# Kernel tuning notes

Hardware: AMD Instinct MI355X
Metric: run time of the kernel (lower is better)

The kernel has to match this reference:

```python
import jax, jax.numpy as jnp
import numpy as np


def _nearest(x, h, w):
    # torch F.interpolate(mode='nearest'): src_idx = floor(dst_idx * in/out)
    Hi, Wi = x.shape[-2], x.shape[-1]
    ri = (jnp.arange(h) * Hi) // h
    ci = (jnp.arange(w) * Wi) // w
    return jnp.take(jnp.take(x, ri, axis=-2), ci, axis=-1)


def _conv2d(x, wgt, bias):
    y = jax.lax.conv_general_dilated(x, wgt, (1, 1), 'SAME',
                                     dimension_numbers=('NCHW', 'OIHW', 'NCHW'))
    return y + bias.reshape(1, -1, 1, 1)


def setup_inputs() -> dict:
    key = jax.random.key(0)
    ks = jax.random.split(key, 6)
    b, c, ref_n, h, w = 1, 128, 4, 64, 64
    Hv, Wv = 256, 256
    return {
        'feats_t': jax.random.normal(ks[0], (b, c, h, w), jnp.float32),
        'feats_ref': jax.random.normal(ks[1], (b, c, ref_n, h, w), jnp.float32),
        'v_t': jax.random.uniform(ks[2], (b, 1, Hv, Wv), dtype=jnp.float32),
        'v_ref': jax.random.uniform(ks[3], (b, 1, ref_n, Hv, Wv), dtype=jnp.float32),
        'conv1_w': jax.random.normal(ks[4], (1, 1, 3, 3), jnp.float32) * 0.1,
        'conv1_b': jnp.zeros((1,), jnp.float32),
        'conv2_w': jax.random.normal(ks[5], (1, 1, 3, 3), jnp.float32) * 0.1,
        'conv2_b': jnp.zeros((1,), jnp.float32),
    }


def reference(feats_t, feats_ref, v_t, v_ref, conv1_w, conv1_b, conv2_w, conv2_b):
    b, c, ref_n, h, w = feats_ref.shape
    # nearest-resize visibility masks to feature resolution
    vt = _nearest(v_t, h, w)                      # (b, 1, h, w)
    vr = _nearest(v_ref, h, w)                    # (b, 1, ref_n, h, w)
    ft = feats_t * vt                             # (b, c, h, w)
    fr = feats_ref * vr                           # (b, c, ref_n, h, w)
    # cost volume: corr[b,r,q,k] = sum_c ft[b,c,q] * fr[b,c,r,k]
    corr = jnp.einsum('bcq,bcrk->brqk',
                      ft.reshape(b, c, h * w),
                      fr.reshape(b, c, ref_n, h * w))
    corr = corr.reshape(b, ref_n, h, w, h, w)
    # separable 4D conv: 3x3 over (h_ref, w_ref), then 3x3 over (h_t, w_t)
    x = _conv2d(corr.reshape(b * ref_n * h * w, 1, h, w), conv1_w, conv1_b)
    x = x.reshape(b, ref_n, h, w, h, w).transpose(0, 1, 4, 5, 2, 3)
    x = _conv2d(x.reshape(b * ref_n * h * w, 1, h, w), conv2_w, conv2_b)
    corr = x.reshape(b, ref_n, h, w, h, w).transpose(0, 1, 4, 5, 2, 3)
    # softmax3d: joint softmax over (ref_n, h_ref, w_ref) per query location
    m = jnp.max(corr, axis=(1, 4, 5), keepdims=True)
    e = jnp.exp(corr - m)
    corr = e / jnp.sum(e, axis=(1, 4, 5), keepdims=True)
    # weighted aggregation: out[b,c,q] = sum_{r,k} fr[b,c,r,k] * corr[b,r,q,k]
    out = jnp.einsum('bcrk,brqk->bcq',
                     fr.reshape(b, c, ref_n, h * w),
                     corr.reshape(b, ref_n, h * w, h * w))
    return out.reshape(b, c, h, w)
```

## Files before the change

kernel.cpp:

```cpp
#include <hip/hip_runtime.h>
#include <stdint.h>
#include <math.h>

typedef short bf16x8 __attribute__((ext_vector_type(8)));
typedef float f32x16 __attribute__((ext_vector_type(16)));
typedef unsigned int uint4v __attribute__((ext_vector_type(4)));

#define GAS __attribute__((address_space(1)))
#define LAS __attribute__((address_space(3)))

#define CDIM 128
#define NQ   4096
#define NK   16384
#define QT   128
#define KTILE 64

__device__ __forceinline__ unsigned short f2bf(float f) {
    unsigned int u = __builtin_bit_cast(unsigned int, f);
    u = (u + 0x7fffu + ((u >> 16) & 1u)) >> 16;
    return (unsigned short)u;
}

__device__ __forceinline__ void gload_lds16(const void* g, void* l) {
    __builtin_amdgcn_global_load_lds((const GAS unsigned int*)g, (LAS unsigned int*)l, 16, 0, 0);
}

__device__ __forceinline__ unsigned cvtpk(float a, float b) {
    unsigned r;
    asm("v_cvt_pk_bf16_f32 %0, %1, %2" : "=v"(r) : "v"(a), "v"(b));
    return r;
}

__device__ __forceinline__ void swap32(unsigned& a, unsigned& b) {
    asm("v_permlane32_swap_b32 %0, %1" : "+v"(a), "+v"(b));
}

__global__ void prep_q_kernel(const float* __restrict__ feats_t,
                              const float* __restrict__ v_t,
                              const float* __restrict__ w2,
                              unsigned int* __restrict__ Q32) {
    int idx = blockIdx.x * 256 + threadIdx.x;
    int q = idx & 4095, cp = idx >> 12;
    int y = q >> 6, x = q & 63;
    const float* fb0 = feats_t + (size_t)(cp * 2) * 4096;
    const float* fb1 = fb0 + 4096;
    float wv[9];
#pragma unroll
    for (int i = 0; i < 9; ++i) wv[i] = w2[i];
    float acc0 = 0.f, acc1 = 0.f;
#pragma unroll
    for (int u = 0; u < 3; ++u) {
        int yy = y + u - 1;
        if ((unsigned)yy >= 64u) continue;
#pragma unroll
        for (int v = 0; v < 3; ++v) {
            int xx = x + v - 1;
            if ((unsigned)xx >= 64u) continue;
            float m = wv[u * 3 + v] * v_t[yy * 1024 + xx * 4];
            acc0 += m * fb0[yy * 64 + xx];
            acc1 += m * fb1[yy * 64 + xx];
        }
    }
    Q32[(size_t)q * 64 + cp] = (unsigned)f2bf(acc0) | ((unsigned)f2bf(acc1) << 16);
}

__global__ void prep_p_kernel(const float* __restrict__ feats_ref,
                              const float* __restrict__ v_ref,
                              float* __restrict__ P,
                              unsigned short* __restrict__ Vt2) {
    int idx = blockIdx.x * 256 + threadIdx.x;
    int c = idx >> 14, rk = idx & 16383;
    int r = rk >> 12, k4 = rk & 4095, ky = k4 >> 6, kx = k4 & 63;
    float v = feats_ref[idx] * v_ref[r * 65536 + ky * 1024 + kx * 4];
    P[idx] = v;
    Vt2[(size_t)(rk >> 6) * 8192 + (((rk >> 3) & 7) * 128 + c) * 8 + (rk & 7)] = f2bf(v);
}

__global__ void prep_k2_kernel(const float* __restrict__ P,
                               const float* __restrict__ w1,
                               unsigned int* __restrict__ K32) {
    int idx = blockIdx.x * 256 + threadIdx.x;
    int rk = idx & 16383, cp2 = idx >> 14;
    int r = rk >> 12, k4 = rk & 4095, ky = k4 >> 6, kx = k4 & 63;
    const float* pb0 = P + (size_t)(cp2 * 2) * NK + r * 4096;
    const float* pb1 = pb0 + NK;
    float wv[9];
#pragma unroll
    for (int i = 0; i < 9; ++i) wv[i] = w1[i];
    float acc0 = 0.f, acc1 = 0.f;
#pragma unroll
    for (int u = 0; u < 3; ++u) {
        int yy = ky + u - 1;
        if ((unsigned)yy >= 64u) continue;
#pragma unroll
        for (int v = 0; v < 3; ++v) {
            int xx = kx + v - 1;
            if ((unsigned)xx >= 64u) continue;
            float w = wv[u * 3 + v];
            acc0 += w * pb0[yy * 64 + xx];
            acc1 += w * pb1[yy * 64 + xx];
        }
    }
    int tile = rk >> 6, rw = rk & 63;
    K32[(size_t)tile * 4096 + ((cp2 >> 2) * 64 + rw) * 4 + (cp2 & 3)] =
        (unsigned)f2bf(acc0) | ((unsigned)f2bf(acc1) << 16);
}

template<int KS>
__launch_bounds__(256, 2)
__global__ void attn_kernel(const unsigned short* __restrict__ Qg,
                            const unsigned short* __restrict__ Kt,
                            const unsigned short* __restrict__ Vt2,
                            float* __restrict__ Opart,
                            float* __restrict__ lpart) {
    constexpr int NITER = (NK / KS) / KTILE;
    __shared__ __align__(16) unsigned short KV[2][2][8192];

    const int tid = threadIdx.x;
    const int wid = tid >> 6;
    const int lane = tid & 63;
    const int l31 = lane & 31;
    const int lh = lane >> 5;
    const int ks = blockIdx.x & (KS - 1);
    const int qt = blockIdx.x / KS;
    const int q0 = qt * QT + wid * 32;
    const int tile0 = ks * NITER;

    bf16x8 qf[8];
#pragma unroll
    for (int s = 0; s < 8; ++s)
        qf[s] = *(const bf16x8*)(Qg + (size_t)(q0 + l31) * CDIM + s * 16 + lh * 8);

    f32x16 accO[4];
#pragma unroll
    for (int u = 0; u < 4; ++u)
#pragma unroll
        for (int r = 0; r < 16; ++r) accO[u][r] = 0.f;
    float l_acc = 0.f;

#define STAGE(nb, tg)                                                             \
    do {                                                                          \
        _Pragma("unroll") for (int j = 0; j < 4; ++j) {                           \
            int mb = (wid * 4 + j) * 64;                                          \
            gload_lds16(Kt + (size_t)(tg) * 8192 + (mb + lane) * 8,               \
                        &KV[(nb)][0][mb * 8]);                                    \
            gload_lds16(Vt2 + (size_t)(tg) * 8192 + (mb + lane) * 8,              \
                        &KV[(nb)][1][mb * 8]);                                    \
        }                                                                         \
    } while (0)

    STAGE(0, tile0);

#pragma unroll 1
    for (int it = 0; it < NITER; ++it) {
        const int bc = it & 1;
        __syncthreads();
        if (it + 1 < NITER) {
            STAGE(bc ^ 1, tile0 + it + 1);
            asm volatile("s_waitcnt vmcnt(8)" ::: "memory");
        } else {
            asm volatile("s_waitcnt vmcnt(0)" ::: "memory");
        }
        __syncthreads();

        f32x16 S0, S1;
#pragma unroll
        for (int r = 0; r < 16; ++r) { S0[r] = 0.f; S1[r] = 0.f; }
        __builtin_amdgcn_s_setprio(1);
#pragma unroll
        for (int s = 0; s < 8; ++s) {
            bf16x8 kf0 = *(const bf16x8*)(&KV[bc][0][((s * 2 + lh) * 64 + l31) * 8]);
            S0 = __builtin_amdgcn_mfma_f32_32x32x16_bf16(kf0, qf[s], S0, 0, 0, 0);
        }
#pragma unroll
        for (int s = 0; s < 8; ++s) {
            bf16x8 kf1 = *(const bf16x8*)(&KV[bc][0][((s * 2 + lh) * 64 + 32 + l31) * 8]);
            S1 = __builtin_amdgcn_mfma_f32_32x32x16_bf16(kf1, qf[s], S1, 0, 0, 0);
        }
        __builtin_amdgcn_s_setprio(0);

        float e0[16];
#pragma unroll
        for (int r = 0; r < 16; ++r) e0[r] = __expf(S0[r]);
        {
            float t0 = (e0[0] + e0[1]) + (e0[2] + e0[3]);
            float t1 = (e0[4] + e0[5]) + (e0[6] + e0[7]);
            float t2 = (e0[8] + e0[9]) + (e0[10] + e0[11]);
            float t3 = (e0[12] + e0[13]) + (e0[14] + e0[15]);
            l_acc += (t0 + t1) + (t2 + t3);
        }
        unsigned a0 = cvtpk(e0[0], e0[1]),   a1 = cvtpk(e0[2], e0[3]);
        unsigned a2 = cvtpk(e0[4], e0[5]),   a3 = cvtpk(e0[6], e0[7]);
        unsigned a4 = cvtpk(e0[8], e0[9]),   a5 = cvtpk(e0[10], e0[11]);
        unsigned a6 = cvtpk(e0[12], e0[13]), a7 = cvtpk(e0[14], e0[15]);
        swap32(a0, a2); swap32(a1, a3); swap32(a4, a6); swap32(a5, a7);
        bf16x8 pA0 = __builtin_bit_cast(bf16x8, (uint4v){a0, a1, a2, a3});
        bf16x8 pB0 = __builtin_bit_cast(bf16x8, (uint4v){a4, a5, a6, a7});

        __builtin_amdgcn_s_setprio(1);
#pragma unroll
        for (int u = 0; u < 4; ++u) {
            bf16x8 v0a = *(const bf16x8*)(&KV[bc][1][((lh) * 128 + u * 32 + l31) * 8]);
            accO[u] = __builtin_amdgcn_mfma_f32_32x32x16_bf16(v0a, pA0, accO[u], 0, 0, 0);
            bf16x8 v0b = *(const bf16x8*)(&KV[bc][1][((2 + lh) * 128 + u * 32 + l31) * 8]);
            accO[u] = __builtin_amdgcn_mfma_f32_32x32x16_bf16(v0b, pB0, accO[u], 0, 0, 0);
        }
        __builtin_amdgcn_s_setprio(0);

        float e1[16];
#pragma unroll
        for (int r = 0; r < 16; ++r) e1[r] = __expf(S1[r]);
        {
            float t0 = (e1[0] + e1[1]) + (e1[2] + e1[3]);
            float t1 = (e1[4] + e1[5]) + (e1[6] + e1[7]);
            float t2 = (e1[8] + e1[9]) + (e1[10] + e1[11]);
            float t3 = (e1[12] + e1[13]) + (e1[14] + e1[15]);
            l_acc += (t0 + t1) + (t2 + t3);
        }
        unsigned b0 = cvtpk(e1[0], e1[1]),   b1 = cvtpk(e1[2], e1[3]);
        unsigned b2 = cvtpk(e1[4], e1[5]),   b3 = cvtpk(e1[6], e1[7]);
        unsigned b4 = cvtpk(e1[8], e1[9]),   b5 = cvtpk(e1[10], e1[11]);
        unsigned b6 = cvtpk(e1[12], e1[13]), b7 = cvtpk(e1[14], e1[15]);
        swap32(b0, b2); swap32(b1, b3); swap32(b4, b6); swap32(b5, b7);
        bf16x8 pA1 = __builtin_bit_cast(bf16x8, (uint4v){b0, b1, b2, b3});
        bf16x8 pB1 = __builtin_bit_cast(bf16x8, (uint4v){b4, b5, b6, b7});

        __builtin_amdgcn_s_setprio(1);
#pragma unroll
        for (int u = 0; u < 4; ++u) {
            bf16x8 v1a = *(const bf16x8*)(&KV[bc][1][((4 + lh) * 128 + u * 32 + l31) * 8]);
            accO[u] = __builtin_amdgcn_mfma_f32_32x32x16_bf16(v1a, pA1, accO[u], 0, 0, 0);
            bf16x8 v1b = *(const bf16x8*)(&KV[bc][1][((6 + lh) * 128 + u * 32 + l31) * 8]);
            accO[u] = __builtin_amdgcn_mfma_f32_32x32x16_bf16(v1b, pB1, accO[u], 0, 0, 0);
        }
        __builtin_amdgcn_s_setprio(0);
    }
#undef STAGE

    l_acc += __shfl_xor(l_acc, 32);
    if (lane < 32) lpart[ks * NQ + q0 + l31] = l_acc;
#pragma unroll
    for (int u = 0; u < 4; ++u)
#pragma unroll
        for (int r = 0; r < 16; ++r) {
            int c = u * 32 + (r & 3) + 8 * (r >> 2) + 4 * lh;
            Opart[((size_t)(ks * CDIM + c)) * NQ + q0 + l31] = accO[u][r];
        }
}

template<int KS>
__global__ void reduce_kernel(const float* __restrict__ Opart,
                              const float* __restrict__ lpart,
                              float* __restrict__ out) {
    int i = blockIdx.x * 256 + threadIdx.x;
    int c = i >> 12, q = i & 4095;
    float den = 0.f, o = 0.f;
#pragma unroll
    for (int s = 0; s < KS; ++s) {
        den += lpart[s * NQ + q];
        o += Opart[((size_t)(s * CDIM + c)) * NQ + q];
    }
    out[(size_t)c * NQ + q] = o / den;
}

extern "C" void kernel_launch(void* const* d_in, const int* in_sizes, int n_in,
                              void* d_out, int out_size, void* d_ws, size_t ws_size,
                              hipStream_t stream) {
    (void)in_sizes; (void)n_in; (void)out_size;
    const float* feats_t   = (const float*)d_in[0];
    const float* feats_ref = (const float*)d_in[1];
    const float* v_t       = (const float*)d_in[2];
    const float* v_ref     = (const float*)d_in[3];
    const float* w1        = (const float*)d_in[4];
    const float* w2        = (const float*)d_in[6];
    float* out = (float*)d_out;

    const size_t opart_off = (size_t)(9u << 20);
    const size_t per_split = (size_t)NQ * CDIM * 4;
    const size_t need16 = opart_off + 16 * per_split + 16 * NQ * 4;
    const size_t need8  = opart_off + 8  * per_split + 8  * NQ * 4;
    if (ws_size < need8) return;

    char* ws = (char*)d_ws;
    unsigned int*   Q   = (unsigned int*)(ws);
    unsigned short* Kt  = (unsigned short*)(ws + (size_t)(1u << 20));
    unsigned short* Vt2 = (unsigned short*)(ws + (size_t)(5u << 20));
    float* Opart = (float*)(ws + opart_off);
    float* P     = Opart;

    hipLaunchKernelGGL(prep_q_kernel, dim3(1024), dim3(256), 0, stream, feats_t, v_t, w2, Q);
    hipLaunchKernelGGL(prep_p_kernel, dim3(8192), dim3(256), 0, stream, feats_ref, v_ref, P, Vt2);
    hipLaunchKernelGGL(prep_k2_kernel, dim3(4096), dim3(256), 0, stream, P, w1, (unsigned int*)Kt);

    if (ws_size >= need16) {
        float* lpart = (float*)(ws + opart_off + 16 * per_split);
        hipLaunchKernelGGL(HIP_KERNEL_NAME(attn_kernel<16>), dim3((NQ / QT) * 16), dim3(256), 0,
                           stream, (const unsigned short*)Q, Kt, Vt2, Opart, lpart);
        hipLaunchKernelGGL(HIP_KERNEL_NAME(reduce_kernel<16>), dim3(2048), dim3(256), 0,
                           stream, Opart, lpart, out);
    } else {
        float* lpart = (float*)(ws + opart_off + 8 * per_split);
        hipLaunchKernelGGL(HIP_KERNEL_NAME(attn_kernel<8>), dim3((NQ / QT) * 8), dim3(256), 0,
                           stream, (const unsigned short*)Q, Kt, Vt2, Opart, lpart);
        hipLaunchKernelGGL(HIP_KERNEL_NAME(reduce_kernel<8>), dim3(2048), dim3(256), 0,
                           stream, Opart, lpart, out);
    }
}
```

Before: 74.39 us.

## Read K/V fragments directly from global memory instead of LDS double-buffering

Removes the shared-memory double-buffered staging of K and V tiles (global_load_lds plus barriers) and has each wave load its MFMA operand fragments straight from global memory. This drops the per-iteration __syncthreads and the LDS footprint, which could raise occupancy. In exchange, all four waves in a block now fetch the same K/V data independently through the caches, and there is no explicit prefetch to hide load latency behind the MFMAs.

```diff
diff --git a/kernel.cpp b/kernel.cpp
--- a/kernel.cpp
+++ b/kernel.cpp
@@ -5,9 +5,6 @@
 typedef short bf16x8 __attribute__((ext_vector_type(8)));
 typedef float f32x16 __attribute__((ext_vector_type(16)));
 typedef unsigned int uint4v __attribute__((ext_vector_type(4)));
-
-#define GAS __attribute__((address_space(1)))
-#define LAS __attribute__((address_space(3)))
 
 #define CDIM 128
 #define NQ   4096
@@ -19,10 +16,6 @@
     unsigned int u = __builtin_bit_cast(unsigned int, f);
     u = (u + 0x7fffu + ((u >> 16) & 1u)) >> 16;
     return (unsigned short)u;
-}
-
-__device__ __forceinline__ void gload_lds16(const void* g, void* l) {
-    __builtin_amdgcn_global_load_lds((const GAS unsigned int*)g, (LAS unsigned int*)l, 16, 0, 0);
 }
 
 __device__ __forceinline__ unsigned cvtpk(float a, float b) {
@@ -114,7 +107,6 @@
                             float* __restrict__ Opart,
                             float* __restrict__ lpart) {
     constexpr int NITER = (NK / KS) / KTILE;
-    __shared__ __align__(16) unsigned short KV[2][2][8192];
 
     const int tid = threadIdx.x;
     const int wid = tid >> 6;
@@ -138,30 +130,10 @@
         for (int r = 0; r < 16; ++r) accO[u][r] = 0.f;
     float l_acc = 0.f;
 
-#define STAGE(nb, tg)                                                             \
-    do {                                                                          \
-        _Pragma("unroll") for (int j = 0; j < 4; ++j) {                           \
-            int mb = (wid * 4 + j) * 64;                                          \
-            gload_lds16(Kt + (size_t)(tg) * 8192 + (mb + lane) * 8,               \
-                        &KV[(nb)][0][mb * 8]);                                    \
-            gload_lds16(Vt2 + (size_t)(tg) * 8192 + (mb + lane) * 8,              \
-                        &KV[(nb)][1][mb * 8]);                                    \
-        }                                                                         \
-    } while (0)
-
-    STAGE(0, tile0);
-
 #pragma unroll 1
     for (int it = 0; it < NITER; ++it) {
-        const int bc = it & 1;
-        __syncthreads();
-        if (it + 1 < NITER) {
-            STAGE(bc ^ 1, tile0 + it + 1);
-            asm volatile("s_waitcnt vmcnt(8)" ::: "memory");
-        } else {
-            asm volatile("s_waitcnt vmcnt(0)" ::: "memory");
-        }
-        __syncthreads();
+        const unsigned short* kb = Kt + (size_t)(tile0 + it) * 8192;
+        const unsigned short* vb = Vt2 + (size_t)(tile0 + it) * 8192;
 
         f32x16 S0, S1;
 #pragma unroll
@@ -169,12 +141,9 @@
         __builtin_amdgcn_s_setprio(1);
 #pragma unroll
         for (int s = 0; s < 8; ++s) {
-            bf16x8 kf0 = *(const bf16x8*)(&KV[bc][0][((s * 2 + lh) * 64 + l31) * 8]);
+            bf16x8 kf0 = *(const bf16x8*)(kb + (size_t)(((s * 2 + lh) * 64 + l31) * 8));
             S0 = __builtin_amdgcn_mfma_f32_32x32x16_bf16(kf0, qf[s], S0, 0, 0, 0);
-        }
-#pragma unroll
-        for (int s = 0; s < 8; ++s) {
-            bf16x8 kf1 = *(const bf16x8*)(&KV[bc][0][((s * 2 + lh) * 64 + 32 + l31) * 8]);
+            bf16x8 kf1 = *(const bf16x8*)(kb + (size_t)(((s * 2 + lh) * 64 + 32 + l31) * 8));
             S1 = __builtin_amdgcn_mfma_f32_32x32x16_bf16(kf1, qf[s], S1, 0, 0, 0);
         }
         __builtin_amdgcn_s_setprio(0);
@@ -200,9 +169,9 @@
         __builtin_amdgcn_s_setprio(1);
 #pragma unroll
         for (int u = 0; u < 4; ++u) {
-            bf16x8 v0a = *(const bf16x8*)(&KV[bc][1][((lh) * 128 + u * 32 + l31) * 8]);
+            bf16x8 v0a = *(const bf16x8*)(vb + (size_t)(((lh) * 128 + u * 32 + l31) * 8));
             accO[u] = __builtin_amdgcn_mfma_f32_32x32x16_bf16(v0a, pA0, accO[u], 0, 0, 0);
-            bf16x8 v0b = *(const bf16x8*)(&KV[bc][1][((2 + lh) * 128 + u * 32 + l31) * 8]);
+            bf16x8 v0b = *(const bf16x8*)(vb + (size_t)(((2 + lh) * 128 + u * 32 + l31) * 8));
             accO[u] = __builtin_amdgcn_mfma_f32_32x32x16_bf16(v0b, pB0, accO[u], 0, 0, 0);
         }
         __builtin_amdgcn_s_setprio(0);
@@ -228,14 +197,13 @@
         __builtin_amdgcn_s_setprio(1);
 #pragma unroll
         for (int u = 0; u < 4; ++u) {
-            bf16x8 v1a = *(const bf16x8*)(&KV[bc][1][((4 + lh) * 128 + u * 32 + l31) * 8]);
+            bf16x8 v1a = *(const bf16x8*)(vb + (size_t)(((4 + lh) * 128 + u * 32 + l31) * 8));
             accO[u] = __builtin_amdgcn_mfma_f32_32x32x16_bf16(v1a, pA1, accO[u], 0, 0, 0);
-            bf16x8 v1b = *(const bf16x8*)(&KV[bc][1][((6 + lh) * 128 + u * 32 + l31) * 8]);
+            bf16x8 v1b = *(const bf16x8*)(vb + (size_t)(((6 + lh) * 128 + u * 32 + l31) * 8));
             accO[u] = __builtin_amdgcn_mfma_f32_32x32x16_bf16(v1b, pB1, accO[u], 0, 0, 0);
         }
         __builtin_amdgcn_s_setprio(0);
     }
-#undef STAGE
 
     l_acc += __shfl_xor(l_acc, 32);
     if (lane < 32) lpart[ks * NQ + q0 + l31] = l_acc;
```

After: 104.9 us. 41.0% more time.
